# Performance work log

Measured on AMD Instinct MI355X. Metric: run time of the kernel, lower is better.

Reference implementation:

```python
import jax, jax.numpy as jnp
import numpy as np

CLASS_NUM = 20
C_FEAT = 256
STRIDE = 16
ROI = 7
SCALE = 1.0 / 16.0
TOPK = 300
NMS_THR = 0.7
SCORE_THR = 0.5
SAMPLES = 2  # nearest samples per bin edge in roi_pool


def _conv(x, W, b, stride, padding):
    y = jax.lax.conv_general_dilated(x, W, (stride, stride), padding,
                                     dimension_numbers=('NCHW', 'OIHW', 'NCHW'))
    return y + b[None, :, None, None]


def _pairwise_iou(boxes):
    x1, y1, x2, y2 = boxes[:, 0], boxes[:, 1], boxes[:, 2], boxes[:, 3]
    area = jnp.maximum(x2 - x1, 0.) * jnp.maximum(y2 - y1, 0.)
    ix1 = jnp.maximum(x1[:, None], x1[None, :])
    iy1 = jnp.maximum(y1[:, None], y1[None, :])
    ix2 = jnp.minimum(x2[:, None], x2[None, :])
    iy2 = jnp.minimum(y2[:, None], y2[None, :])
    inter = jnp.maximum(ix2 - ix1, 0.) * jnp.maximum(iy2 - iy1, 0.)
    return inter / jnp.maximum(area[:, None] + area[None, :] - inter, 1e-6)


def _nms(boxes, scores, valid, thr):
    # fixed-size greedy NMS: returns boolean keep mask aligned with input order
    K = boxes.shape[0]
    order = jnp.argsort(-scores)
    b = boxes[order]
    v = valid[order]
    iou = _pairwise_iou(b)  # [K,K]
    idx = jnp.arange(K)

    def body(i, keep):
        k = keep[i] & v[i]
        suppress = (iou[i] > thr) & (idx > i) & k
        return keep & (~suppress)

    keep = jax.lax.fori_loop(0, K, body, v)
    return jnp.zeros((K,), bool).at[order].set(keep)


def _roi_pool(f, boxes):
    # f: [C,H,W] feature map; boxes: [K,4] in image coords.
    # Max pool over ROI x SAMPLES nearest-neighbor samples per bin (jit-safe roi_pool).
    C, H, W = f.shape
    K = boxes.shape[0]
    b = boxes * SCALE
    frac = (jnp.arange(ROI)[:, None] + (jnp.arange(SAMPLES)[None, :] + 0.5) / SAMPLES).reshape(-1) / ROI
    xs = b[:, 0:1] + frac[None, :] * (b[:, 2:3] - b[:, 0:1])  # [K, ROI*S]
    ys = b[:, 1:2] + frac[None, :] * (b[:, 3:4] - b[:, 1:2])
    ix = jnp.clip(jnp.floor(xs), 0, W - 1).astype(jnp.int32)
    iy = jnp.clip(jnp.floor(ys), 0, H - 1).astype(jnp.int32)
    g = f[:, iy[:, :, None], ix[:, None, :]]  # [C,K,ROI*S,ROI*S]
    g = g.reshape(C, K, ROI, SAMPLES, ROI, SAMPLES)
    return g.max(axis=(3, 5)).transpose(1, 0, 2, 3)  # [K,C,ROI,ROI]


def setup_inputs() -> dict:
    key = jax.random.key(0)
    ks = jax.random.split(key, 12)
    img = 800
    x = jax.random.uniform(ks[0], (1, 3, img, img), jnp.float32)
    gt_boxes = jax.random.uniform(ks[1], (8, 5), jnp.float32) * img

    def w_(k, shape, fan_in):
        return jax.random.normal(k, shape, jnp.float32) * (1.0 / np.sqrt(fan_in))

    d_flat = ROI * ROI * C_FEAT
    return {
        'x': x, 'gt_boxes': gt_boxes,
        'W_feat': w_(ks[2], (C_FEAT, 3, STRIDE, STRIDE), 3 * STRIDE * STRIDE),
        'b_feat': jnp.zeros((C_FEAT,), jnp.float32),
        'W1': w_(ks[3], (C_FEAT, C_FEAT, 3, 3), C_FEAT * 9),
        'b1': jnp.zeros((C_FEAT,), jnp.float32),
        'Wc': w_(ks[4], (2, C_FEAT), C_FEAT),
        'bc': jnp.zeros((2,), jnp.float32),
        'Wb': w_(ks[5], (4, C_FEAT), C_FEAT),
        'bb': jnp.zeros((4,), jnp.float32),
        'fc1_w': w_(ks[6], (4096, d_flat), d_flat),
        'fc1_b': jnp.zeros((4096,), jnp.float32),
        'fc2_w': w_(ks[7], (4096, 4096), 4096),
        'fc2_b': jnp.zeros((4096,), jnp.float32),
        'cls_w': w_(ks[8], (CLASS_NUM + 1, 4096), 4096),
        'cls_b': jnp.zeros((CLASS_NUM + 1,), jnp.float32),
        'box_w': w_(ks[9], (4, 4096), 4096),
        'box_b': jnp.zeros((4,), jnp.float32),
        'w': 800, 'h': 800,
    }


def reference(x, gt_boxes, W_feat, b_feat, W1, b1, Wc, bc, Wb, bb,
              fc1_w, fc1_b, fc2_w, fc2_b, cls_w, cls_b, box_w, box_b, w, h):
    feature = _conv(x, W_feat, b_feat, STRIDE, 'VALID')          # [1,C,50,50]
    hmap = jax.nn.relu(_conv(feature, W1, b1, 1, 'SAME'))
    pre_labels = (jnp.einsum('nchw,oc->nhwo', hmap, Wc) + bc).reshape(-1, 2)
    pre_boxes = (jnp.einsum('nchw,oc->nhwo', hmap, Wb) + bb).reshape(-1, 4)
    logits = jax.nn.softmax(pre_labels, axis=-1)[:, 1]           # [2500]
    scores, idx = jax.lax.top_k(logits, TOPK)                    # fixed-size stand-in for score>thr select
    valid = scores > SCORE_THR
    pb = pre_boxes[idx]
    wf = jnp.float32(w)
    hf = jnp.float32(h)
    # box decode exactly as the original per-box loop (vectorized)
    x1 = jnp.maximum(pb[:, 2] - pb[:, 0] / 2, 0.)
    y1 = jnp.maximum(pb[:, 3] - pb[:, 1] / 2, 0.)
    x2 = jnp.minimum(pb[:, 2] + pb[:, 0], wf)
    y2 = jnp.minimum(pb[:, 3] + pb[:, 1], hf)
    boxes = jnp.stack([x1, y1, x2, y2], axis=-1)                 # [K,4]
    keep = _nms(boxes, scores, valid, NMS_THR)
    pooled = _roi_pool(feature[0], boxes)                        # [K,C,7,7]
    flat = pooled.reshape(TOPK, -1)
    h1 = jax.nn.relu(flat @ fc1_w.T + fc1_b)
    h2 = jax.nn.relu(h1 @ fc2_w.T + fc2_b)
    cls = h2 @ cls_w.T + cls_b                                   # [K,21]
    box = h2 @ box_w.T + box_b                                   # [K,4]
    out = jnp.where(keep[:, None], jnp.concatenate([cls, box], axis=-1), 0.)
    return out                                                   # [K,25]
```

## Files before the change

### kernel.cpp

```cpp
#include <hip/hip_runtime.h>
#include <hip/hip_bf16.h>
#include <math.h>

#define NPIX   2500
#define CFEAT  256
#define NTOP   300
#define DFLAT  12544
#define FCN    4096
#define FPSTRIDE 3328
#define KG1    392
#define KG2    128
#define MT     20

typedef _Float16 f16x8 __attribute__((ext_vector_type(8)));
typedef float    f32x4 __attribute__((ext_vector_type(4)));

static constexpr size_t OFF_FPAD  = 0;
static constexpr size_t OFF_SCORE = 0x5C0000;
static constexpr size_t OFF_PREB  = 0x5D0000;
static constexpr size_t OFF_KEEP  = 0x5E5000;
static constexpr size_t OFF_IX    = 0x5E6000;
static constexpr size_t OFF_IY    = 0x5EB000;
static constexpr size_t OFF_AFRAG = 0x600000;
static constexpr size_t OFF_H1F   = 0xE00000;
static constexpr size_t OFF_H2    = 0x1100000;
static constexpr size_t OFF_W1T   = 0x1600000;
static constexpr size_t OFF_PART  = 0x1900000;

__device__ inline float decode_dim(const void* p) {
    int iv = *(const int*)p;
    if (iv > 0 && iv < (1 << 20)) return (float)iv;
    return __int_as_float(iv);
}

__global__ void zero_fpad(float* __restrict__ fpad) {
    int i = blockIdx.x * 256 + threadIdx.x;
    if (i < 212992) *(float4*)(fpad + (size_t)i * 4) = make_float4(0.f, 0.f, 0.f, 0.f);
}

__global__ void __launch_bounds__(256)
patch_conv(const float* __restrict__ x, const float* __restrict__ Wf,
           const float* __restrict__ bf, float* __restrict__ fpad) {
    __shared__ float w[3072];
    int co0 = blockIdx.y * 4;
    for (int t = threadIdx.x; t < 3072; t += 256) w[t] = Wf[co0 * 768 + t];
    __syncthreads();
    int p = blockIdx.x * 256 + threadIdx.x;
    if (p >= NPIX) return;
    int py = p / 50, px = p % 50;
    float acc[4];
    #pragma unroll
    for (int c = 0; c < 4; ++c) acc[c] = bf[co0 + c];
    for (int ci = 0; ci < 3; ++ci) {
        const float* xp = x + ci * 640000 + (py * 16) * 800 + px * 16;
        #pragma unroll
        for (int ky = 0; ky < 16; ++ky) {
            const float* row = xp + ky * 800;
            #pragma unroll
            for (int kq = 0; kq < 4; ++kq) {
                float4 xv = *reinterpret_cast<const float4*>(row + kq * 4);
                int kb = ci * 256 + ky * 16 + kq * 4;
                #pragma unroll
                for (int c = 0; c < 4; ++c) {
                    const float* wc = w + c * 768 + kb;
                    acc[c] += xv.x * wc[0] + xv.y * wc[1] + xv.z * wc[2] + xv.w * wc[3];
                }
            }
        }
    }
    size_t o = (size_t)(py + 1) * 64 + (px + 1);
    #pragma unroll
    for (int c = 0; c < 4; ++c) fpad[(size_t)(co0 + c) * FPSTRIDE + o] = acc[c];
}

__global__ void transpose_w1(const float* __restrict__ W1, float* __restrict__ W1t) {
    int idx = blockIdx.x * 256 + threadIdx.x;
    if (idx >= 2304 * 256) return;
    int r = idx >> 8, co = idx & 255;
    W1t[idx] = W1[co * 2304 + r];
}

__global__ void __launch_bounds__(256)
conv3x3_part(const float* __restrict__ fpad, const float* __restrict__ W1t,
             float* __restrict__ cpart, int zci) {
    int co = threadIdx.x;
    int xb = blockIdx.x * 8;
    int y  = blockIdx.y;
    int z  = blockIdx.z;
    float acc[8];
    #pragma unroll
    for (int p = 0; p < 8; ++p) acc[p] = 0.0f;
    const float* fp = fpad + (size_t)(z * zci) * FPSTRIDE + (size_t)y * 64 + xb;
    const float* wp = W1t + (size_t)(z * zci) * 9 * 256 + co;
    #pragma unroll 2
    for (int ci = 0; ci < zci; ++ci) {
        float v[3][12];
        #pragma unroll
        for (int dy = 0; dy < 3; ++dy) {
            #pragma unroll
            for (int q = 0; q < 3; ++q) {
                float4 r4 = *(const float4*)(fp + dy * 64 + q * 4);
                v[dy][q * 4 + 0] = r4.x; v[dy][q * 4 + 1] = r4.y;
                v[dy][q * 4 + 2] = r4.z; v[dy][q * 4 + 3] = r4.w;
            }
        }
        float wv[9];
        #pragma unroll
        for (int k = 0; k < 9; ++k) wv[k] = wp[k * 256];
        #pragma unroll
        for (int dy = 0; dy < 3; ++dy)
            #pragma unroll
            for (int dx = 0; dx < 3; ++dx) {
                float wvv = wv[dy * 3 + dx];
                #pragma unroll
                for (int p = 0; p < 8; ++p)
                    acc[p] += v[dy][p + dx] * wvv;
            }
        fp += FPSTRIDE;
        wp += 9 * 256;
    }
    size_t base = (size_t)z * (NPIX * 256) + (size_t)(y * 50 + xb) * 256 + co;
    #pragma unroll
    for (int p = 0; p < 8; ++p)
        if (xb + p < 50) cpart[base + (size_t)p * 256] = acc[p];
}

__global__ void __launch_bounds__(256)
reducehead_k(const float* __restrict__ cpart, const float* __restrict__ b1,
             const float* __restrict__ Wc, const float* __restrict__ bc,
             const float* __restrict__ Wb, const float* __restrict__ bb,
             float* __restrict__ score, float* __restrict__ preb, int zs) {
    int lane = threadIdx.x & 63;
    int p = blockIdx.x * 4 + (threadIdx.x >> 6);
    if (p >= NPIX) return;
    size_t off = (size_t)p * 256 + lane * 4;
    float4 h = *(const float4*)(cpart + off);
    for (int z = 1; z < zs; ++z) {
        float4 v = *(const float4*)(cpart + (size_t)z * (NPIX * 256) + off);
        h.x += v.x; h.y += v.y; h.z += v.z; h.w += v.w;
    }
    float4 b = *(const float4*)(b1 + lane * 4);
    h.x = fmaxf(h.x + b.x, 0.f); h.y = fmaxf(h.y + b.y, 0.f);
    h.z = fmaxf(h.z + b.z, 0.f); h.w = fmaxf(h.w + b.w, 0.f);
    float4 c0 = *(const float4*)(Wc + lane * 4);
    float4 c1 = *(const float4*)(Wc + 256 + lane * 4);
    float4 w0 = *(const float4*)(Wb + lane * 4);
    float4 w1 = *(const float4*)(Wb + 256 + lane * 4);
    float4 w2 = *(const float4*)(Wb + 512 + lane * 4);
    float4 w3 = *(const float4*)(Wb + 768 + lane * 4);
    float s[6];
    s[0] = h.x*c0.x + h.y*c0.y + h.z*c0.z + h.w*c0.w;
    s[1] = h.x*c1.x + h.y*c1.y + h.z*c1.z + h.w*c1.w;
    s[2] = h.x*w0.x + h.y*w0.y + h.z*w0.z + h.w*w0.w;
    s[3] = h.x*w1.x + h.y*w1.y + h.z*w1.z + h.w*w1.w;
    s[4] = h.x*w2.x + h.y*w2.y + h.z*w2.z + h.w*w2.w;
    s[5] = h.x*w3.x + h.y*w3.y + h.z*w3.z + h.w*w3.w;
    #pragma unroll
    for (int o = 1; o < 64; o <<= 1) {
        #pragma unroll
        for (int q = 0; q < 6; ++q) s[q] += __shfl_xor(s[q], o, 64);
    }
    if (lane == 0) {
        float s0 = s[0] + bc[0], s1 = s[1] + bc[1];
        float m = fmaxf(s0, s1);
        float e0 = expf(s0 - m), e1 = expf(s1 - m);
        score[p] = e1 / (e0 + e1);
        preb[p * 4 + 0] = s[2] + bb[0];
        preb[p * 4 + 1] = s[3] + bb[1];
        preb[p * 4 + 2] = s[4] + bb[2];
        preb[p * 4 + 3] = s[5] + bb[3];
    }
}

__global__ void __launch_bounds__(1024)
topknms_k(const float* __restrict__ score, const float* __restrict__ preb,
          const void* wp_, const void* hp_, int* __restrict__ keep,
          int* __restrict__ ixb, int* __restrict__ iyb) {
    __shared__ unsigned long long KEYS[NPIX];
    __shared__ unsigned int hist[256];
    __shared__ int sh_digit, sh_newr, cnt;
    __shared__ unsigned long long SEL[NTOP];
    __shared__ unsigned long long SORT[NTOP];
    __shared__ float X1[320], Y1[320], X2[320], Y2[320], AR[320];
    __shared__ unsigned long long MASK[320][5];
    __shared__ unsigned long long KEEPW[5];
    int tid = threadIdx.x;
    int lane = tid & 63;
    int w = tid >> 6;

    for (int e = tid; e < NPIX; e += 1024) {
        unsigned sb = __float_as_uint(score[e]);
        KEYS[e] = ((unsigned long long)sb << 32) | (unsigned)(~e);
    }
    if (tid == 0) cnt = 0;
    __syncthreads();

    unsigned long long P = 0ull, M = 0ull;
    int r = NTOP;
    for (int pass = 0; pass < 8; ++pass) {
        int shift = 56 - 8 * pass;
        if (tid < 256) hist[tid] = 0u;
        __syncthreads();
        for (int e = tid; e < NPIX; e += 1024) {
            unsigned long long k = KEYS[e];
            if ((k & M) == P)
                atomicAdd(&hist[(unsigned)(k >> shift) & 255u], 1u);
        }
        __syncthreads();
        if (tid < 64) {
            unsigned c0 = hist[tid * 4 + 0], c1 = hist[tid * 4 + 1];
            unsigned c2 = hist[tid * 4 + 2], c3 = hist[tid * 4 + 3];
            unsigned sl = c0 + c1 + c2 + c3;
            unsigned suf = sl;
            #pragma unroll
            for (int off = 1; off < 64; off <<= 1) {
                unsigned o = __shfl_down(suf, off, 64);
                if (lane + off < 64) suf += o;
            }
            unsigned G = suf - sl;
            if (G < (unsigned)r && G + sl >= (unsigned)r) {
                unsigned above = G;
                unsigned cc[4] = {c0, c1, c2, c3};
                int d = 0; unsigned ab = above;
                #pragma unroll
                for (int i = 3; i >= 0; --i) {
                    if (ab < (unsigned)r && ab + cc[i] >= (unsigned)r) { d = tid * 4 + i; break; }
                    ab += cc[i];
                }
                sh_digit = d;
                sh_newr = r - (int)ab;
            }
        }
        __syncthreads();
        P |= ((unsigned long long)(unsigned)sh_digit) << shift;
        M |= 0xFFull << shift;
        r = sh_newr;
    }
    unsigned long long T = P;

    for (int e = tid; e < NPIX; e += 1024) {
        unsigned long long k = KEYS[e];
        if (k >= T) {
            int s = atomicAdd(&cnt, 1);
            SEL[s] = k;
        }
    }
    __syncthreads();

    if (tid < NTOP) {
        unsigned long long mine = SEL[tid];
        int rank = 0;
        for (int j = 0; j < NTOP; ++j) rank += (SEL[j] > mine) ? 1 : 0;
        SORT[rank] = mine;
    }
    __syncthreads();

    if (tid < 320) {
        float x1 = 0.f, y1 = 0.f, x2 = 0.f, y2 = 0.f;
        bool v = false;
        if (tid < NTOP) {
            unsigned long long key = SORT[tid];
            int id = (int)(~(unsigned)key);
            float sc = __uint_as_float((unsigned)(key >> 32));
            float wf = decode_dim(wp_), hf = decode_dim(hp_);
            float p0 = preb[id * 4 + 0], p1 = preb[id * 4 + 1];
            float p2 = preb[id * 4 + 2], p3 = preb[id * 4 + 3];
            x1 = fmaxf(p2 - p0 * 0.5f, 0.0f);
            y1 = fmaxf(p3 - p1 * 0.5f, 0.0f);
            x2 = fminf(p2 + p0, wf);
            y2 = fminf(p3 + p1, hf);
            v = sc > 0.5f;
            float bx1 = x1 * 0.0625f, by1 = y1 * 0.0625f;
            float bx2 = x2 * 0.0625f, by2 = y2 * 0.0625f;
            #pragma unroll
            for (int m = 0; m < 14; ++m) {
                int i = m >> 1, s = m & 1;
                float frac = ((float)i + (s ? 0.75f : 0.25f)) / 7.0f;
                float xs = bx1 + frac * (bx2 - bx1);
                float ys = by1 + frac * (by2 - by1);
                float fx = floorf(xs); fx = fminf(fmaxf(fx, 0.0f), 49.0f);
                float fy = floorf(ys); fy = fminf(fmaxf(fy, 0.0f), 49.0f);
                ixb[tid * 14 + m] = (int)fx;
                iyb[tid * 14 + m] = (int)fy;
            }
        }
        X1[tid] = x1; Y1[tid] = y1; X2[tid] = x2; Y2[tid] = y2;
        AR[tid] = fmaxf(x2 - x1, 0.0f) * fmaxf(y2 - y1, 0.0f);
        unsigned long long vb = __ballot(v);
        if (lane == 0 && w < 5) KEEPW[w] = vb;
    }
    __syncthreads();

    if (tid < 320) {
        float xi1 = X1[tid], yi1 = Y1[tid], xi2 = X2[tid], yi2 = Y2[tid], ai = AR[tid];
        #pragma unroll
        for (int jw = 0; jw < 5; ++jw) {
            unsigned long long mword = 0ull;
            #pragma unroll 4
            for (int j2 = 0; j2 < 64; ++j2) {
                int j = jw * 64 + j2;
                float ix1 = fmaxf(xi1, X1[j]);
                float iy1 = fmaxf(yi1, Y1[j]);
                float ix2 = fminf(xi2, X2[j]);
                float iy2 = fminf(yi2, Y2[j]);
                float inter = fmaxf(ix2 - ix1, 0.0f) * fmaxf(iy2 - iy1, 0.0f);
                float iou = inter / fmaxf(ai + AR[j] - inter, 1e-6f);
                bool sup = (iou > 0.7f) && (j > tid) && (j < NTOP);
                mword |= sup ? (1ull << j2) : 0ull;
            }
            MASK[tid][jw] = mword;
        }
    }
    __syncthreads();

    if (tid < 64) {
        unsigned long long m[5][5];
        #pragma unroll
        for (int g = 0; g < 5; ++g)
            #pragma unroll
            for (int q = 0; q < 5; ++q)
                m[g][q] = MASK[g * 64 + lane][q];
        unsigned long long kw0 = KEEPW[0], kw1 = KEEPW[1], kw2 = KEEPW[2],
                           kw3 = KEEPW[3], kw4 = KEEPW[4];
        #pragma unroll
        for (int g = 0; g < 5; ++g) {
            for (int i2 = 0; i2 < 64; ++i2) {
                unsigned long long kg = (g == 0) ? kw0 : (g == 1) ? kw1 :
                                        (g == 2) ? kw2 : (g == 3) ? kw3 : kw4;
                bool alive = (kg >> i2) & 1ull;
                unsigned long long b0 = __shfl(m[g][0], i2, 64);
                unsigned long long b1 = __shfl(m[g][1], i2, 64);
                unsigned long long b2 = __shfl(m[g][2], i2, 64);
                unsigned long long b3 = __shfl(m[g][3], i2, 64);
                unsigned long long b4 = __shfl(m[g][4], i2, 64);
                if (alive) {
                    kw0 &= ~b0; kw1 &= ~b1; kw2 &= ~b2; kw3 &= ~b3; kw4 &= ~b4;
                }
            }
        }
        #pragma unroll
        for (int g = 0; g < 5; ++g) {
            unsigned long long kg = (g == 0) ? kw0 : (g == 1) ? kw1 :
                                    (g == 2) ? kw2 : (g == 3) ? kw3 : kw4;
            int j = g * 64 + lane;
            if (j < NTOP) keep[j] = (int)((kg >> lane) & 1ull);
        }
    }
}

__global__ void __launch_bounds__(256)
roipool_frag(const float* __restrict__ fpad, const int* __restrict__ ixb,
             const int* __restrict__ iyb, _Float16* __restrict__ Af) {
    int wid = blockIdx.x * 256 + threadIdx.x;
    if (wid >= MT * KG1 * 64) return;
    int l = wid & 63;
    int g = (wid >> 6) % KG1;
    int T = wid / (KG1 * 64);
    int mm = T * 16 + (l & 15);
    int kbase = g * 32 + ((l >> 4) & 3) * 8;
    union { _Float16 h[8]; uint4 u; } o;
    if (mm < NTOP) {
        const int* ix = ixb + mm * 14;
        const int* iy = iyb + mm * 14;
        #pragma unroll
        for (int e = 0; e < 8; ++e) {
            int k = kbase + e;
            int c = k / 49, ij = k % 49, i = ij / 7, jx = ij % 7;
            int y0 = iy[2 * i] + 1, y1 = iy[2 * i + 1] + 1;
            int x0 = ix[2 * jx] + 1, x1 = ix[2 * jx + 1] + 1;
            const float* f = fpad + (size_t)c * FPSTRIDE;
            float v = fmaxf(fmaxf(f[y0 * 64 + x0], f[y0 * 64 + x1]),
                            fmaxf(f[y1 * 64 + x0], f[y1 * 64 + x1]));
            o.h[e] = (_Float16)v;
        }
    } else {
        o.u.x = 0u; o.u.y = 0u; o.u.z = 0u; o.u.w = 0u;
    }
    *(uint4*)(Af + (size_t)wid * 8) = o.u;
}

__global__ void __launch_bounds__(512)
gemm_fullm(const _Float16* __restrict__ Af, const float* __restrict__ B,
           float* __restrict__ part, int K, int KG, int kchunk) {
    __shared__ char Bs[2][64 * 128];
    int tid = threadIdx.x;
    int lane = tid & 63;
    int w = tid >> 6;
    int wm = w & 3, wn = w >> 2;
    int n0 = blockIdx.x * 64;
    int ks = blockIdx.y * kchunk;
    int nt = kchunk >> 6;

    f32x4 acc[5][2];
    #pragma unroll
    for (int tm = 0; tm < 5; ++tm)
        #pragma unroll
        for (int tn = 0; tn < 2; ++tn)
            acc[tm][tn] = f32x4{0.f, 0.f, 0.f, 0.f};

    int srow = tid >> 3;
    int skp  = (tid & 7) * 8;
    const float* bsrc = B + (size_t)(n0 + srow) * K + ks + skp;
    int sboff = srow * 128 + ((skp * 2) ^ ((srow & 7) << 4));

    float4 v0 = *(const float4*)(bsrc);
    float4 v1 = *(const float4*)(bsrc + 4);
    {
        union { _Float16 h[8]; uint4 u; } cv;
        cv.h[0] = (_Float16)v0.x; cv.h[1] = (_Float16)v0.y;
        cv.h[2] = (_Float16)v0.z; cv.h[3] = (_Float16)v0.w;
        cv.h[4] = (_Float16)v1.x; cv.h[5] = (_Float16)v1.y;
        cv.h[6] = (_Float16)v1.z; cv.h[7] = (_Float16)v1.w;
        *(uint4*)(Bs[0] + sboff) = cv.u;
    }
    if (nt > 1) {
        v0 = *(const float4*)(bsrc + 64);
        v1 = *(const float4*)(bsrc + 68);
    }
    __syncthreads();

    for (int k0 = 0; k0 < nt; ++k0) {
        const char* cur = Bs[k0 & 1];
        if (k0 + 1 < nt) {
            union { _Float16 h[8]; uint4 u; } cv;
            cv.h[0] = (_Float16)v0.x; cv.h[1] = (_Float16)v0.y;
            cv.h[2] = (_Float16)v0.z; cv.h[3] = (_Float16)v0.w;
            cv.h[4] = (_Float16)v1.x; cv.h[5] = (_Float16)v1.y;
            cv.h[6] = (_Float16)v1.z; cv.h[7] = (_Float16)v1.w;
            *(uint4*)(Bs[(k0 + 1) & 1] + sboff) = cv.u;
            if (k0 + 2 < nt) {
                v0 = *(const float4*)(bsrc + (k0 + 2) * 64);
                v1 = *(const float4*)(bsrc + (k0 + 2) * 64 + 4);
            }
        }
        #pragma unroll
        for (int kk = 0; kk < 2; ++kk) {
            int g = (ks + k0 * 64 + kk * 32) >> 5;
            f16x8 bfr[2];
            #pragma unroll
            for (int tn = 0; tn < 2; ++tn) {
                int row = wn * 32 + tn * 16 + (lane & 15);
                int kb = kk * 64 + (lane >> 4) * 16;
                bfr[tn] = *(const f16x8*)(cur + row * 128 + (kb ^ ((row & 7) << 4)));
            }
            #pragma unroll
            for (int tm = 0; tm < 5; ++tm) {
                int T = wm * 5 + tm;
                f16x8 a = *(const f16x8*)(Af + ((size_t)(T * KG + g) * 64 + lane) * 8);
                #pragma unroll
                for (int tn = 0; tn < 2; ++tn)
                    acc[tm][tn] = __builtin_amdgcn_mfma_f32_16x16x32_f16(a, bfr[tn], acc[tm][tn], 0, 0, 0);
            }
        }
        __syncthreads();
    }
    float* pout = part + (size_t)blockIdx.y * (NTOP * FCN);
    #pragma unroll
    for (int tm = 0; tm < 5; ++tm) {
        int mbase = (wm * 5 + tm) * 16 + (lane >> 4) * 4;
        #pragma unroll
        for (int j = 0; j < 4; ++j) {
            int m = mbase + j;
            if (m < NTOP) {
                #pragma unroll
                for (int tn = 0; tn < 2; ++tn) {
                    int n = n0 + wn * 32 + tn * 16 + (lane & 15);
                    pout[(size_t)m * FCN + n] = acc[tm][tn][j];
                }
            }
        }
    }
}

__global__ void reduce_fc1(const float* __restrict__ part, const float* __restrict__ bias,
                           _Float16* __restrict__ h1f, int ns) {
    int i = blockIdx.x * 256 + threadIdx.x;
    if (i >= NTOP * 512) return;
    int m = i >> 9;
    int f = (i & 511) * 8;
    float s[8];
    const float* p0 = part + (size_t)m * FCN + f;
    #pragma unroll
    for (int e = 0; e < 8; ++e) s[e] = p0[e];
    for (int z = 1; z < ns; ++z) {
        const float* pz = p0 + (size_t)z * (NTOP * FCN);
        #pragma unroll
        for (int e = 0; e < 8; ++e) s[e] += pz[e];
    }
    union { _Float16 h[8]; uint4 u; } o;
    #pragma unroll
    for (int e = 0; e < 8; ++e) o.h[e] = (_Float16)fmaxf(s[e] + bias[f + e], 0.0f);
    int T = m >> 4, g = f >> 5, l = (m & 15) + 16 * ((f >> 3) & 3);
    *(uint4*)(h1f + ((size_t)(T * KG2 + g) * 64 + l) * 8) = o.u;
}

__global__ void reduce_fc2(const float* __restrict__ part, const float* __restrict__ bias,
                           float* __restrict__ outp, int ns) {
    size_t i = (size_t)blockIdx.x * 256 + threadIdx.x;
    size_t mn4 = (size_t)NTOP * FCN / 4;
    if (i >= mn4) return;
    float4 s = *(const float4*)(part + i * 4);
    for (int zz = 1; zz < ns; ++zz) {
        float4 v = *(const float4*)(part + (size_t)zz * (NTOP * FCN) + i * 4);
        s.x += v.x; s.y += v.y; s.z += v.z; s.w += v.w;
    }
    int n = (int)((i * 4) % FCN);
    float4 b = *(const float4*)(bias + n);
    s.x = fmaxf(s.x + b.x, 0.f); s.y = fmaxf(s.y + b.y, 0.f);
    s.z = fmaxf(s.z + b.z, 0.f); s.w = fmaxf(s.w + b.w, 0.f);
    *(float4*)(outp + i * 4) = s;
}

__global__ void __launch_bounds__(256)
final_k(const float* __restrict__ h2, const float* __restrict__ clsw,
        const float* __restrict__ clsb, const float* __restrict__ boxw,
        const float* __restrict__ boxb, const int* __restrict__ keep,
        float* __restrict__ out) {
    int gid = blockIdx.x * 4 + (threadIdx.x >> 6);
    if (gid >= NTOP * 25) return;
    int lane = threadIdx.x & 63;
    int k = gid / 25, o = gid % 25;
    const float* w;
    float b;
    if (o < 21) { w = clsw + (size_t)o * 4096; b = clsb[o]; }
    else        { w = boxw + (size_t)(o - 21) * 4096; b = boxb[o - 21]; }
    const float* h = h2 + (size_t)k * 4096;
    float s = 0.0f;
    #pragma unroll
    for (int i = 0; i < 16; ++i) {
        float4 hv = *(const float4*)(h + (i * 64 + lane) * 4);
        float4 wv = *(const float4*)(w + (i * 64 + lane) * 4);
        s += hv.x * wv.x + hv.y * wv.y + hv.z * wv.z + hv.w * wv.w;
    }
    #pragma unroll
    for (int off = 1; off < 64; off <<= 1) s += __shfl_xor(s, off, 64);
    if (lane == 0) out[gid] = keep[k] ? (s + b) : 0.0f;
}

extern "C" void kernel_launch(void* const* d_in, const int* in_sizes, int n_in,
                              void* d_out, int out_size, void* d_ws, size_t ws_size,
                              hipStream_t stream) {
    const float* x    = (const float*)d_in[0];
    const float* Wf   = (const float*)d_in[2];
    const float* bf   = (const float*)d_in[3];
    const float* W1   = (const float*)d_in[4];
    const float* b1   = (const float*)d_in[5];
    const float* Wc   = (const float*)d_in[6];
    const float* bc   = (const float*)d_in[7];
    const float* Wb   = (const float*)d_in[8];
    const float* bb   = (const float*)d_in[9];
    const float* fc1w = (const float*)d_in[10];
    const float* fc1b = (const float*)d_in[11];
    const float* fc2w = (const float*)d_in[12];
    const float* fc2b = (const float*)d_in[13];
    const float* clsw = (const float*)d_in[14];
    const float* clsb = (const float*)d_in[15];
    const float* boxw = (const float*)d_in[16];
    const float* boxb = (const float*)d_in[17];
    const void*  wp   = d_in[18];
    const void*  hp   = d_in[19];

    char* ws = (char*)d_ws;
    float*     fpad  = (float*)(ws + OFF_FPAD);
    float*     score = (float*)(ws + OFF_SCORE);
    float*     preb  = (float*)(ws + OFF_PREB);
    int*       keep  = (int*)(ws + OFF_KEEP);
    int*       ixb   = (int*)(ws + OFF_IX);
    int*       iyb   = (int*)(ws + OFF_IY);
    _Float16*  Af    = (_Float16*)(ws + OFF_AFRAG);
    _Float16*  h1f   = (_Float16*)(ws + OFF_H1F);
    float*     h2    = (float*)(ws + OFF_H2);
    float*     w1t   = (float*)(ws + OFF_W1T);
    float*     out   = (float*)d_out;

    size_t slot = (size_t)NTOP * FCN * 4;
    size_t avail = ws_size > OFF_PART ? (ws_size - OFF_PART) / slot : 0;
    int ns1 = (avail >= 7) ? 7 : (avail >= 4) ? 4 : (avail >= 2) ? 2 : 1;
    int ns2 = (avail >= 4) ? 4 : (avail >= 2) ? 2 : 1;
    float* part1 = (avail >= 1) ? (float*)(ws + OFF_PART) : h2;
    float* part2 = (avail >= 1) ? (float*)(ws + OFF_PART) : (float*)Af;
    int kch1 = (196 / ns1) * 64;
    int kch2 = (64 / ns2) * 64;
    int zs = (avail >= 5) ? 8 : 4;
    float* cpart = (avail >= 5) ? (float*)(ws + OFF_PART) : (float*)(ws + OFF_AFRAG);

    zero_fpad<<<832, 256, 0, stream>>>(fpad);
    patch_conv<<<dim3(10, 64), 256, 0, stream>>>(x, Wf, bf, fpad);
    transpose_w1<<<(2304 * 256 + 255) / 256, 256, 0, stream>>>(W1, w1t);
    conv3x3_part<<<dim3(7, 50, zs), 256, 0, stream>>>(fpad, w1t, cpart, 256 / zs);
    reducehead_k<<<625, 256, 0, stream>>>(cpart, b1, Wc, bc, Wb, bb, score, preb, zs);
    topknms_k<<<1, 1024, 0, stream>>>(score, preb, wp, hp, keep, ixb, iyb);
    roipool_frag<<<(MT * KG1 * 64 + 255) / 256, 256, 0, stream>>>(fpad, ixb, iyb, Af);
    gemm_fullm<<<dim3(64, ns1), 512, 0, stream>>>(Af, fc1w, part1, DFLAT, KG1, kch1);
    reduce_fc1<<<(NTOP * 512 + 255) / 256, 256, 0, stream>>>(part1, fc1b, h1f, ns1);
    gemm_fullm<<<dim3(64, ns2), 512, 0, stream>>>(h1f, fc2w, part2, FCN, KG2, kch2);
    reduce_fc2<<<(NTOP * FCN / 4 + 255) / 256, 256, 0, stream>>>(part2, fc2b, h2, ns2);
    final_k<<<(NTOP * 25 + 3) / 4, 256, 0, stream>>>(h2, clsw, clsb, boxw, boxb, keep, out);
}
```

Before: 357.8 us.

## Widen FC GEMM tiles to 128 columns with 1024-thread blocks and rebalanced split-K

The FC1 and FC2 GEMM kernel now uses 1024-thread workgroups, each covering a 128-column N tile with a doubled shared-memory B buffer. The split-K index is folded into a 1D grid. Uneven K chunks are handled through a per-block `klen`, and both GEMMs now use the same split count of up to 8. The A and B fragments for both 32-wide K halves are loaded before the MFMA chain so load latency can overlap. The aim is more reuse of each staged B tile and of the A fragments per block, at the cost of fewer, larger blocks and higher register pressure under the 1024-thread launch bound.

```diff
diff --git a/kernel.cpp b/kernel.cpp
--- a/kernel.cpp
+++ b/kernel.cpp
@@ -219,9 +219,8 @@
             }
             unsigned G = suf - sl;
             if (G < (unsigned)r && G + sl >= (unsigned)r) {
-                unsigned above = G;
                 unsigned cc[4] = {c0, c1, c2, c3};
-                int d = 0; unsigned ab = above;
+                int d = 0; unsigned ab = G;
                 #pragma unroll
                 for (int i = 3; i >= 0; --i) {
                     if (ab < (unsigned)r && ab + cc[i] >= (unsigned)r) { d = tid * 4 + i; break; }
@@ -379,17 +378,20 @@
     *(uint4*)(Af + (size_t)wid * 8) = o.u;
 }
 
-__global__ void __launch_bounds__(512)
+__global__ void __launch_bounds__(1024)
 gemm_fullm(const _Float16* __restrict__ Af, const float* __restrict__ B,
-           float* __restrict__ part, int K, int KG, int kchunk) {
-    __shared__ char Bs[2][64 * 128];
+           float* __restrict__ part, int K, int KG, int kchunk, int ns) {
+    __shared__ char Bs[2][128 * 128];
     int tid = threadIdx.x;
     int lane = tid & 63;
     int w = tid >> 6;
     int wm = w & 3, wn = w >> 2;
-    int n0 = blockIdx.x * 64;
-    int ks = blockIdx.y * kchunk;
-    int nt = kchunk >> 6;
+    int wg = blockIdx.x;
+    int kz = wg % ns;
+    int n0 = (wg / ns) * 128;
+    int ks = kz * kchunk;
+    int klen = K - ks; if (klen > kchunk) klen = kchunk;
+    int nt = klen >> 6;
 
     f32x4 acc[5][2];
     #pragma unroll
@@ -433,28 +435,32 @@
                 v1 = *(const float4*)(bsrc + (k0 + 2) * 64 + 4);
             }
         }
-        #pragma unroll
-        for (int kk = 0; kk < 2; ++kk) {
-            int g = (ks + k0 * 64 + kk * 32) >> 5;
-            f16x8 bfr[2];
+        int g0 = (ks + k0 * 64) >> 5;
+        f16x8 a0[5], a1[5];
+        #pragma unroll
+        for (int tm = 0; tm < 5; ++tm) {
+            int T = wm * 5 + tm;
+            a0[tm] = *(const f16x8*)(Af + ((size_t)(T * KG + g0) * 64 + lane) * 8);
+            a1[tm] = *(const f16x8*)(Af + ((size_t)(T * KG + g0 + 1) * 64 + lane) * 8);
+        }
+        f16x8 b0[2], b1[2];
+        #pragma unroll
+        for (int tn = 0; tn < 2; ++tn) {
+            int row = wn * 32 + tn * 16 + (lane & 15);
+            int kb0 = (lane >> 4) * 16;
+            b0[tn] = *(const f16x8*)(cur + row * 128 + (kb0 ^ ((row & 7) << 4)));
+            b1[tn] = *(const f16x8*)(cur + row * 128 + ((kb0 + 64) ^ ((row & 7) << 4)));
+        }
+        #pragma unroll
+        for (int tm = 0; tm < 5; ++tm)
             #pragma unroll
             for (int tn = 0; tn < 2; ++tn) {
-                int row = wn * 32 + tn * 16 + (lane & 15);
-                int kb = kk * 64 + (lane >> 4) * 16;
-                bfr[tn] = *(const f16x8*)(cur + row * 128 + (kb ^ ((row & 7) << 4)));
-            }
-            #pragma unroll
-            for (int tm = 0; tm < 5; ++tm) {
-                int T = wm * 5 + tm;
-                f16x8 a = *(const f16x8*)(Af + ((size_t)(T * KG + g) * 64 + lane) * 8);
-                #pragma unroll
-                for (int tn = 0; tn < 2; ++tn)
-                    acc[tm][tn] = __builtin_amdgcn_mfma_f32_16x16x32_f16(a, bfr[tn], acc[tm][tn], 0, 0, 0);
-            }
-        }
+                acc[tm][tn] = __builtin_amdgcn_mfma_f32_16x16x32_f16(a0[tm], b0[tn], acc[tm][tn], 0, 0, 0);
+                acc[tm][tn] = __builtin_amdgcn_mfma_f32_16x16x32_f16(a1[tm], b1[tn], acc[tm][tn], 0, 0, 0);
+            }
         __syncthreads();
     }
-    float* pout = part + (size_t)blockIdx.y * (NTOP * FCN);
+    float* pout = part + (size_t)kz * (NTOP * FCN);
     #pragma unroll
     for (int tm = 0; tm < 5; ++tm) {
         int mbase = (wm * 5 + tm) * 16 + (lane >> 4) * 4;
@@ -575,12 +581,12 @@
 
     size_t slot = (size_t)NTOP * FCN * 4;
     size_t avail = ws_size > OFF_PART ? (ws_size - OFF_PART) / slot : 0;
-    int ns1 = (avail >= 7) ? 7 : (avail >= 4) ? 4 : (avail >= 2) ? 2 : 1;
-    int ns2 = (avail >= 4) ? 4 : (avail >= 2) ? 2 : 1;
+    int ns1 = (avail >= 8) ? 8 : (avail >= 4) ? 4 : (avail >= 2) ? 2 : 1;
+    int ns2 = ns1;
     float* part1 = (avail >= 1) ? (float*)(ws + OFF_PART) : h2;
     float* part2 = (avail >= 1) ? (float*)(ws + OFF_PART) : (float*)Af;
-    int kch1 = (196 / ns1) * 64;
-    int kch2 = (64 / ns2) * 64;
+    int st1 = (196 + ns1 - 1) / ns1;  int kch1 = st1 * 64;  int ns1e = (196 + st1 - 1) / st1;
+    int st2 = (64 + ns2 - 1) / ns2;   int kch2 = st2 * 64;  int ns2e = (64 + st2 - 1) / st2;
     int zs = (avail >= 5) ? 8 : 4;
     float* cpart = (avail >= 5) ? (float*)(ws + OFF_PART) : (float*)(ws + OFF_AFRAG);
 
@@ -591,9 +597,9 @@
     reducehead_k<<<625, 256, 0, stream>>>(cpart, b1, Wc, bc, Wb, bb, score, preb, zs);
     topknms_k<<<1, 1024, 0, stream>>>(score, preb, wp, hp, keep, ixb, iyb);
     roipool_frag<<<(MT * KG1 * 64 + 255) / 256, 256, 0, stream>>>(fpad, ixb, iyb, Af);
-    gemm_fullm<<<dim3(64, ns1), 512, 0, stream>>>(Af, fc1w, part1, DFLAT, KG1, kch1);
-    reduce_fc1<<<(NTOP * 512 + 255) / 256, 256, 0, stream>>>(part1, fc1b, h1f, ns1);
-    gemm_fullm<<<dim3(64, ns2), 512, 0, stream>>>(h1f, fc2w, part2, FCN, KG2, kch2);
-    reduce_fc2<<<(NTOP * FCN / 4 + 255) / 256, 256, 0, stream>>>(part2, fc2b, h2, ns2);
+    gemm_fullm<<<32 * ns1e, 1024, 0, stream>>>(Af, fc1w, part1, DFLAT, KG1, kch1, ns1e);
+    reduce_fc1<<<(NTOP * 512 + 255) / 256, 256, 0, stream>>>(part1, fc1b, h1f, ns1e);
+    gemm_fullm<<<32 * ns2e, 1024, 0, stream>>>(h1f, fc2w, part2, FCN, KG2, kch2, ns2e);
+    reduce_fc2<<<(NTOP * FCN / 4 + 255) / 256, 256, 0, stream>>>(part2, fc2b, h2, ns2e);
     final_k<<<(NTOP * 25 + 3) / 4, 256, 0, stream>>>(h2, clsw, clsb, boxw, boxb, keep, out);
 }
```

After: 345.9 us. 3.3% less time.
